# Optimization experiments

Measured on AMD Instinct MI355X. Metric: run time of the kernel, lower is better.

The kernel has to match this reference:

```python
import jax, jax.numpy as jnp
import numpy as np

EPS = 1e-18
MARGIN = 0.2  # hp.margin (cancels: positive/positive == 1)
BIAS = 1.0    # hp.bias


def setup_inputs() -> dict:
    key = jax.random.key(0)
    k1, k2, k3, k4 = jax.random.split(key, 4)
    B, T, D = 32, 256, 256  # T == D required by the broadcast in Ecos_sim
    return {
        "pre_VF": jax.random.normal(k1, (B, T, D), dtype=jnp.float32),
        "pre_AF": jax.random.normal(k2, (B, T, D), dtype=jnp.float32),
        "back_VF": jax.random.normal(k3, (B, T, D), dtype=jnp.float32),
        "back_AF": jax.random.normal(k4, (B, T, D), dtype=jnp.float32),
    }


def _direction_loss(V, A):
    """For each anchor i: log(1 + sum_{j != i} exp(sim(V_i, A_j))).

    sim(V_i, A_j)[t, s] = (V_i @ A_j.T)[t, s] / (||V_i||_F * colnorm(A_j)[s])
    (faithful to Ecos_sim: scalar Frobenius norm for V, per-column norm for A,
    broadcast along the last axis; positive/positive == 1 exactly, so the
    positive term and margin cancel.)
    """
    B = V.shape[0]
    # upper[i,j,t,s] = <V[i,t,:], A[j,s,:]>
    upper = jnp.einsum("itd,jsd->ijts", V, A)
    v_norm = jnp.sqrt(jnp.sum(V ** 2, axis=(1, 2)) + EPS)      # [B]
    a_norm = jnp.sqrt(jnp.sum(A ** 2, axis=1) + EPS)           # [B, D]
    sim = upper / (v_norm[:, None, None, None] * a_norm[None, :, None, :])
    e_sim = jnp.exp(sim)                                        # [B,B,T,T]
    idx = jnp.arange(B)
    down = e_sim.sum(axis=1) - e_sim[idx, idx]                  # exclude j == i
    rows = jnp.log(1.0 + down)                                  # [B,T,T]
    return rows.reshape(-1, rows.shape[-1])                     # cat along dim 0


def reference(pre_VF, pre_AF, back_VF, back_AF):
    sim_back_V = _direction_loss(back_VF, back_AF)
    sim_back_A = _direction_loss(back_AF, back_VF)
    return -(1.0 / BIAS) * (sim_back_V + sim_back_A)
```

## Files before the change

### kernel.cpp

```cpp
#include <hip/hip_runtime.h>
#include <cstdint>

#define R_TOT 8192
#define KD    256
#define SLOT  ((size_t)R_TOT * KD)
#define IVN_OFF  0
#define ICN_OFF  256
#define CSQ_OFF  (ICN_OFF + 65536)
#define MATS_OFF (CSQ_OFF + 524288)

typedef float f32x4 __attribute__((ext_vector_type(4)));
typedef int   i32x4 __attribute__((ext_vector_type(4)));
typedef int   i32x8 __attribute__((ext_vector_type(8)));

__device__ __forceinline__ void glds16(const void* g, void* l){
  __builtin_amdgcn_global_load_lds((const __attribute__((address_space(1))) uint32_t*)g,
                                   (__attribute__((address_space(3))) uint32_t*)l, 16, 0, 0);
}

__global__ void cast_ns_k(const float* __restrict__ V, const float* __restrict__ A,
                          unsigned char* __restrict__ mats, float* __restrict__ csq){
  const int tc = blockIdx.x, j = blockIdx.y, ten = blockIdx.z;
  const int tid = threadIdx.x;
  const int g    = tid & 31;
  const int tsub = tid >> 5;
  const int c    = g >> 1;
  const int half = g & 1;
  const float* X = (ten ? A : V) + (size_t)j * 65536;
  unsigned char* M = mats + (size_t)ten * SLOT + (size_t)j * 65536;
  float cs[8];
  #pragma unroll
  for (int e = 0; e < 8; ++e) cs[e] = 0.f;
  #pragma unroll
  for (int tt = 0; tt < 4; ++tt){
    const int t = tc * 32 + tt * 8 + tsub;
    const float4 p0 = *(const float4*)(X + t * 256 + g * 8);
    const float4 p1 = *(const float4*)(X + t * 256 + g * 8 + 4);
    cs[0] += p0.x * p0.x; cs[1] += p0.y * p0.y; cs[2] += p0.z * p0.z; cs[3] += p0.w * p0.w;
    cs[4] += p1.x * p1.x; cs[5] += p1.y * p1.y; cs[6] += p1.z * p1.z; cs[7] += p1.w * p1.w;
    int d0 = __builtin_amdgcn_cvt_pk_fp8_f32(p0.x, p0.y, 0, false);
    d0     = __builtin_amdgcn_cvt_pk_fp8_f32(p0.z, p0.w, d0, true);
    int d1 = __builtin_amdgcn_cvt_pk_fp8_f32(p1.x, p1.y, 0, false);
    d1     = __builtin_amdgcn_cvt_pk_fp8_f32(p1.z, p1.w, d1, true);
    int2 o; o.x = d0; o.y = d1;
    *(int2*)(M + (size_t)t * 256 + (((c ^ (t & 15)) << 4) | (half << 3))) = o;
  }
  __shared__ float red[8][256];
  #pragma unroll
  for (int e = 0; e < 8; ++e) red[tsub][g * 8 + e] = cs[e];
  __syncthreads();
  float s = 0.f;
  #pragma unroll
  for (int gg = 0; gg < 8; ++gg) s += red[gg][tid];
  csq[(size_t)((tc * 2 + ten) * 32 + j) * 256 + tid] = s;
}

__global__ void nreduce_k(const float* __restrict__ csq, float* __restrict__ ivn,
                          float* __restrict__ icn){
  const int j = blockIdx.x, ten = blockIdx.y, s = threadIdx.x;
  float c = 0.f;
  #pragma unroll
  for (int tc = 0; tc < 8; ++tc)
    c += csq[(size_t)((tc * 2 + ten) * 32 + j) * 256 + s];
  icn[ten * 8192 + j * 256 + s] = rsqrtf(c + 1e-18f);
  __shared__ float red[256];
  red[s] = c; __syncthreads();
  for (int off = 128; off > 0; off >>= 1){
    if (s < off) red[s] += red[s + off];
    __syncthreads();
  }
  if (s == 0) ivn[ten * 32 + j] = rsqrtf(red[0] + 1e-18f);
}

__global__ __launch_bounds__(512, 4) void gemm_both_k(const unsigned char* __restrict__ mats,
                                                      const float* __restrict__ ivn,
                                                      const float* __restrict__ icn,
                                                      float* __restrict__ out){
  __shared__ __align__(16) char smem[69632];
  const int tid  = threadIdx.x;
  const int lane = tid & 63;
  const int w    = tid >> 6;
  const int dir  = w >> 2;
  const int sub  = w & 3;
  const int lm   = lane & 15;
  const int kh   = lane >> 4;
  const int s0   = blockIdx.x * 16;
  const int rb   = blockIdx.y;
  const int r0   = rb * 256;
  const int ib   = rb;

  const unsigned char* rowmat = mats + (size_t)dir * SLOT;
  const unsigned char* colmat = mats + (size_t)(1 - dir) * SLOT;
  const float sivn = ivn[dir * 32 + ib] * 1.44269504088896340736f;

  char*  dbase = smem + dir * 32768;
  float* cscw  = (float*)(smem + 65536) + dir * 512;
  const unsigned char* colbase = colmat + (size_t)s0 * 256;
  const int lo16 = lane * 16;

  auto issue = [&](int x){
    const int j = x + (x >= ib ? 1 : 0);
    glds16(colbase + (size_t)j * 65536 + sub * 1024 + lo16,
           dbase + ((x & 7) << 12) + sub * 1024 + lo16);
  };

  issue(0); issue(1); issue(2); issue(3);

  {
    const float* ib2 = icn + (size_t)(1 - dir) * 8192 + s0 + lm;
    #pragma unroll
    for (int jx = 0; jx < 2; ++jx){
      const int j = sub * 8 + jx * 4 + kh;
      cscw[j * 16 + lm] = sivn * ib2[j * 256];
    }
  }

  i32x8 afr[4][2];
  #pragma unroll
  for (int mi = 0; mi < 4; ++mi){
    const unsigned char* rp = rowmat + (size_t)(r0 + sub * 64 + mi * 16 + lm) * 256;
    #pragma unroll
    for (int t = 0; t < 2; ++t){
      i32x4 lo = *(const i32x4*)(rp + ((((t << 3) | (kh << 1) | 0) ^ lm) << 4));
      i32x4 hi = *(const i32x4*)(rp + ((((t << 3) | (kh << 1) | 1) ^ lm) << 4));
      afr[mi][t] = i32x8{lo.x, lo.y, lo.z, lo.w, hi.x, hi.y, hi.z, hi.w};
    }
  }
  #pragma unroll
  for (int mi = 0; mi < 4; ++mi)
    #pragma unroll
    for (int t = 0; t < 2; ++t)
      asm volatile("" : "+v"(afr[mi][t]));

  int ad[2][2];
  #pragma unroll
  for (int t = 0; t < 2; ++t)
    #pragma unroll
    for (int u = 0; u < 2; ++u)
      ad[t][u] = lm * 256 + ((((t << 3) | (kh << 1) | u) ^ lm) << 4);

  f32x4 acc[4];
  #pragma unroll
  for (int mi = 0; mi < 4; ++mi)
    acc[mi] = f32x4{0.f, 0.f, 0.f, 0.f};
  const f32x4 fz = {0.f, 0.f, 0.f, 0.f};

  asm volatile("s_waitcnt vmcnt(0) lgkmcnt(0)" ::: "memory");
  __builtin_amdgcn_s_barrier();
  __builtin_amdgcn_sched_barrier(0);

#define RD(RX, BUF) do{                                                         \
    i32x4 lo0_ = *(const i32x4*)((BUF) + ad[0][0]);                             \
    i32x4 hi0_ = *(const i32x4*)((BUF) + ad[0][1]);                             \
    i32x4 lo1_ = *(const i32x4*)((BUF) + ad[1][0]);                             \
    i32x4 hi1_ = *(const i32x4*)((BUF) + ad[1][1]);                             \
    RX[0] = i32x8{lo0_.x, lo0_.y, lo0_.z, lo0_.w, hi0_.x, hi0_.y, hi0_.z, hi0_.w}; \
    RX[1] = i32x8{lo1_.x, lo1_.y, lo1_.z, lo1_.w, hi1_.x, hi1_.y, hi1_.z, hi1_.w}; \
  }while(0)

#define MFMA8(SX, BX) do{                                                       \
    _Pragma("unroll")                                                           \
    for (int mi_ = 0; mi_ < 4; ++mi_)                                           \
      SX[mi_] = __builtin_amdgcn_mfma_scale_f32_16x16x128_f8f6f4(afr[mi_][0], BX[0], fz, 0, 0, 0, 127, 0, 127); \
    _Pragma("unroll")                                                           \
    for (int mi_ = 0; mi_ < 4; ++mi_)                                           \
      SX[mi_] = __builtin_amdgcn_mfma_scale_f32_16x16x128_f8f6f4(afr[mi_][1], BX[1], SX[mi_], 0, 0, 0, 127, 0, 127); \
  }while(0)

#define EXPACC(SX, CY) do{                                                      \
    _Pragma("unroll")                                                           \
    for (int mi_ = 0; mi_ < 4; ++mi_){                                          \
      const f32x4 t_ = SX[mi_] * (CY);                                          \
      f32x4 e_;                                                                 \
      _Pragma("unroll")                                                         \
      for (int r_ = 0; r_ < 4; ++r_) e_[r_] = __builtin_amdgcn_exp2f(t_[r_]);   \
      acc[mi_] += e_;                                                           \
    }                                                                           \
  }while(0)

#define PAIRSEQ(xa_, xb_, NISS, VN) do{                                         \
    const int ja_ = (xa_) + ((xa_) >= ib ? 1 : 0);                              \
    const int jb_ = (xb_) + ((xb_) >= ib ? 1 : 0);                              \
    i32x8 r_[2];                                                                \
    f32x4 S_[4];                                                                \
    RD(r_, dbase + (((xa_) & 7) << 12));                                        \
    const float cA_ = cscw[ja_ * 16 + lm];                                      \
    if ((NISS) >= 1) issue((xa_) + 4);                                          \
    if ((NISS) >= 2) issue((xb_) + 4);                                          \
    MFMA8(S_, r_);                                                              \
    EXPACC(S_, cA_);                                                            \
    __builtin_amdgcn_sched_barrier(0);                                          \
    RD(r_, dbase + (((xb_) & 7) << 12));                                        \
    const float cB_ = cscw[jb_ * 16 + lm];                                      \
    MFMA8(S_, r_);                                                              \
    EXPACC(S_, cB_);                                                            \
    asm volatile("s_waitcnt vmcnt(" #VN ")" ::: "memory");                      \
    __builtin_amdgcn_s_barrier();                                               \
    __builtin_amdgcn_sched_barrier(0);                                          \
  }while(0)

  #pragma unroll 1
  for (int k = 0; k < 13; ++k)
    PAIRSEQ(2 * k, 2 * k + 1, 2, 2);
  PAIRSEQ(26, 27, 1, 1);
  PAIRSEQ(28, 29, 0, 0);
  {
    const int j30 = 30 + (30 >= ib ? 1 : 0);
    i32x8 r_[2];
    f32x4 S_[4];
    RD(r_, dbase + ((30 & 7) << 12));
    const float c_ = cscw[j30 * 16 + lm];
    MFMA8(S_, r_);
    EXPACC(S_, c_);
  }

#undef PAIRSEQ
#undef EXPACC
#undef MFMA8
#undef RD

  __syncthreads();
  float* ebuf = (float*)smem;
  #pragma unroll
  for (int mi = 0; mi < 4; ++mi){
    #pragma unroll
    for (int r = 0; r < 4; ++r){
      const int m = sub * 64 + mi * 16 + (kh << 2) + r;
      ebuf[(dir * 256 + m) * 20 + lm] = __logf(1.f + acc[mi][r]);
    }
  }
  __syncthreads();
  #pragma unroll
  for (int p = 0; p < 2; ++p){
    const int i   = tid + p * 512;
    const int row = i >> 2;
    const int c4  = i & 3;
    const f32x4 e0 = *(const f32x4*)(&ebuf[row * 20 + c4 * 4]);
    const f32x4 e1 = *(const f32x4*)(&ebuf[(256 + row) * 20 + c4 * 4]);
    f32x4 o;
    #pragma unroll
    for (int e = 0; e < 4; ++e) o[e] = -(e0[e] + e1[e]);
    *(f32x4*)(&out[(size_t)(r0 + row) * 256 + s0 + c4 * 4]) = o;
  }
}

extern "C" void kernel_launch(void* const* d_in, const int* in_sizes, int n_in,
                              void* d_out, int out_size, void* d_ws, size_t ws_size,
                              hipStream_t stream){
  const float* V = (const float*)d_in[2];
  const float* A = (const float*)d_in[3];
  float* out = (float*)d_out;
  float* ivn = (float*)((char*)d_ws + IVN_OFF);
  float* icn = (float*)((char*)d_ws + ICN_OFF);
  float* csq = (float*)((char*)d_ws + CSQ_OFF);
  unsigned char* mats = (unsigned char*)((char*)d_ws + MATS_OFF);

  cast_ns_k<<<dim3(8, 32, 2), 256, 0, stream>>>(V, A, mats, csq);
  nreduce_k<<<dim3(32, 2), 256, 0, stream>>>(csq, ivn, icn);
  gemm_both_k<<<dim3(16, 32), 512, 0, stream>>>(mats, ivn, icn, out);
}
```

Baseline: 118.5 us.

## Restructure tile pipeline into four-tile windows with one barrier each

Replaces the paired-tile schedule with windows of four tiles. Each window first issues the global-to-LDS loads for the next four tiles, computes the current four, then waits for all loads and hits one barrier. This halves the number of workgroup barriers and deepens the prefetch from two tiles to four, using the existing 8-slot LDS ring. The trade-off is a full vmcnt(0) drain at each window boundary instead of a partial wait, which can expose load latency if the four tiles of compute do not cover it.

```diff
diff --git a/kernel.cpp b/kernel.cpp
--- a/kernel.cpp
+++ b/kernel.cpp
@@ -149,28 +149,29 @@
   __builtin_amdgcn_s_barrier();
   __builtin_amdgcn_sched_barrier(0);
 
-#define RD(RX, BUF) do{                                                         \
-    i32x4 lo0_ = *(const i32x4*)((BUF) + ad[0][0]);                             \
-    i32x4 hi0_ = *(const i32x4*)((BUF) + ad[0][1]);                             \
-    i32x4 lo1_ = *(const i32x4*)((BUF) + ad[1][0]);                             \
-    i32x4 hi1_ = *(const i32x4*)((BUF) + ad[1][1]);                             \
-    RX[0] = i32x8{lo0_.x, lo0_.y, lo0_.z, lo0_.w, hi0_.x, hi0_.y, hi0_.z, hi0_.w}; \
-    RX[1] = i32x8{lo1_.x, lo1_.y, lo1_.z, lo1_.w, hi1_.x, hi1_.y, hi1_.z, hi1_.w}; \
-  }while(0)
-
-#define MFMA8(SX, BX) do{                                                       \
+#define TILE(x_) do{                                                            \
+    const int j_ = (x_) + ((x_) >= ib ? 1 : 0);                                 \
+    const char* rbuf_ = dbase + (((x_) & 7) << 12);                             \
+    i32x8 b_[2];                                                                \
+    {                                                                           \
+      i32x4 lo0 = *(const i32x4*)(rbuf_ + ad[0][0]);                            \
+      i32x4 hi0 = *(const i32x4*)(rbuf_ + ad[0][1]);                            \
+      i32x4 lo1 = *(const i32x4*)(rbuf_ + ad[1][0]);                            \
+      i32x4 hi1 = *(const i32x4*)(rbuf_ + ad[1][1]);                            \
+      b_[0] = i32x8{lo0.x, lo0.y, lo0.z, lo0.w, hi0.x, hi0.y, hi0.z, hi0.w};    \
+      b_[1] = i32x8{lo1.x, lo1.y, lo1.z, lo1.w, hi1.x, hi1.y, hi1.z, hi1.w};    \
+    }                                                                           \
+    const float csc_ = cscw[j_ * 16 + lm];                                      \
+    f32x4 S_[4];                                                                \
     _Pragma("unroll")                                                           \
     for (int mi_ = 0; mi_ < 4; ++mi_)                                           \
-      SX[mi_] = __builtin_amdgcn_mfma_scale_f32_16x16x128_f8f6f4(afr[mi_][0], BX[0], fz, 0, 0, 0, 127, 0, 127); \
+      S_[mi_] = __builtin_amdgcn_mfma_scale_f32_16x16x128_f8f6f4(afr[mi_][0], b_[0], fz, 0, 0, 0, 127, 0, 127); \
     _Pragma("unroll")                                                           \
     for (int mi_ = 0; mi_ < 4; ++mi_)                                           \
-      SX[mi_] = __builtin_amdgcn_mfma_scale_f32_16x16x128_f8f6f4(afr[mi_][1], BX[1], SX[mi_], 0, 0, 0, 127, 0, 127); \
-  }while(0)
-
-#define EXPACC(SX, CY) do{                                                      \
+      S_[mi_] = __builtin_amdgcn_mfma_scale_f32_16x16x128_f8f6f4(afr[mi_][1], b_[1], S_[mi_], 0, 0, 0, 127, 0, 127); \
     _Pragma("unroll")                                                           \
     for (int mi_ = 0; mi_ < 4; ++mi_){                                          \
-      const f32x4 t_ = SX[mi_] * (CY);                                          \
+      const f32x4 t_ = S_[mi_] * csc_;                                          \
       f32x4 e_;                                                                 \
       _Pragma("unroll")                                                         \
       for (int r_ = 0; r_ < 4; ++r_) e_[r_] = __builtin_amdgcn_exp2f(t_[r_]);   \
@@ -178,46 +179,26 @@
     }                                                                           \
   }while(0)
 
-#define PAIRSEQ(xa_, xb_, NISS, VN) do{                                         \
-    const int ja_ = (xa_) + ((xa_) >= ib ? 1 : 0);                              \
-    const int jb_ = (xb_) + ((xb_) >= ib ? 1 : 0);                              \
-    i32x8 r_[2];                                                                \
-    f32x4 S_[4];                                                                \
-    RD(r_, dbase + (((xa_) & 7) << 12));                                        \
-    const float cA_ = cscw[ja_ * 16 + lm];                                      \
-    if ((NISS) >= 1) issue((xa_) + 4);                                          \
-    if ((NISS) >= 2) issue((xb_) + 4);                                          \
-    MFMA8(S_, r_);                                                              \
-    EXPACC(S_, cA_);                                                            \
-    __builtin_amdgcn_sched_barrier(0);                                          \
-    RD(r_, dbase + (((xb_) & 7) << 12));                                        \
-    const float cB_ = cscw[jb_ * 16 + lm];                                      \
-    MFMA8(S_, r_);                                                              \
-    EXPACC(S_, cB_);                                                            \
-    asm volatile("s_waitcnt vmcnt(" #VN ")" ::: "memory");                      \
-    __builtin_amdgcn_s_barrier();                                               \
-    __builtin_amdgcn_sched_barrier(0);                                          \
-  }while(0)
-
   #pragma unroll 1
-  for (int k = 0; k < 13; ++k)
-    PAIRSEQ(2 * k, 2 * k + 1, 2, 2);
-  PAIRSEQ(26, 27, 1, 1);
-  PAIRSEQ(28, 29, 0, 0);
-  {
-    const int j30 = 30 + (30 >= ib ? 1 : 0);
-    i32x8 r_[2];
-    f32x4 S_[4];
-    RD(r_, dbase + ((30 & 7) << 12));
-    const float c_ = cscw[j30 * 16 + lm];
-    MFMA8(S_, r_);
-    EXPACC(S_, c_);
-  }
-
-#undef PAIRSEQ
-#undef EXPACC
-#undef MFMA8
-#undef RD
+  for (int wnd = 0; wnd < 7; ++wnd){
+    const int base = wnd * 4;
+    issue(base + 4);
+    issue(base + 5);
+    if (base + 6 <= 30) issue(base + 6);
+    if (base + 7 <= 30) issue(base + 7);
+    TILE(base + 0);
+    TILE(base + 1);
+    TILE(base + 2);
+    TILE(base + 3);
+    asm volatile("s_waitcnt vmcnt(0)" ::: "memory");
+    __builtin_amdgcn_s_barrier();
+    __builtin_amdgcn_sched_barrier(0);
+  }
+  TILE(28);
+  TILE(29);
+  TILE(30);
+
+#undef TILE
 
   __syncthreads();
   float* ebuf = (float*)smem;
```

New measurement: 117.3 us. No clear change (-1.0%).
